# Performance work log

Hardware: AMD Instinct MI355X
Metric: run time of the kernel (lower is better)

The kernel has to match this reference:

```python
import jax, jax.numpy as jnp
import numpy as np

MASS, CHARGE, ALPHA, BETA = 1.0, 0.5, 0.1, 0.05
ETA = jnp.array([1.0, -1.0, -1.0, -1.0], dtype=jnp.float32)  # Minkowski metric diag


def setup_inputs() -> dict:
    key = jax.random.key(0)
    k1, k2, k3 = jax.random.split(key, 3)
    B = 262144
    y = jax.random.normal(k1, (B, 8), dtype=jnp.float32)
    W = jax.random.normal(k2, (4, 4), dtype=jnp.float32) * 0.3
    V = jax.random.normal(k3, (4, 4), dtype=jnp.float32) * 0.3
    return {"y": y, "W": W, "V": V}


def _lagrangian(z):
    # z = (x, u, A) concatenated, shape [12]
    x, u, A = z[0:4], z[4:8], z[8:12]
    kinetic = 0.5 * MASS * jnp.sum(ETA * u * u)
    coupling = CHARGE * jnp.sum(ETA * u * A)
    xu_term = ALPHA * jnp.sum((x * u) ** 2)      # makes J_xu nontrivial
    uA_term = BETA * jnp.sum(u * A) ** 2          # makes J_Au nontrivial
    return kinetic + coupling + xu_term + uA_term


def reference(y, W, V):
    def A_vec(x):  # vector potential A^mu(x), works on [4] or [B,4]
        return jnp.tanh(x @ W.T) + x @ V.T

    x = y[:, 0:4]   # [B,4] positions
    u = y[:, 4:8]   # [B,4] velocities
    A = A_vec(x)    # [B,4]
    z = jnp.concatenate([x, u, A], axis=1)  # [B,12] = (x,u,A)

    gradL = jax.vmap(jax.grad(_lagrangian))(z)      # [B,12]
    H = jax.vmap(jax.hessian(_lagrangian))(z)       # [B,12,12]

    dL_dx = gradL[:, 0:4]
    dL_dA = gradL[:, 8:12]
    J_xu = H[:, 0:4, 4:8]    # d^2L/(dx^mu du^nu)
    J_uu = H[:, 4:8, 4:8]    # d^2L/(du^mu du^nu)
    J_Au = H[:, 8:12, 4:8]   # d^2L/(dA^mu du^nu)

    # dA_dx[a, nu, i] = dA^i/dx^nu (matches tf.stack(..., axis=2) layout)
    jacA = jax.vmap(jax.jacfwd(A_vec))(x)           # [B, i, nu]
    dA_dx = jnp.transpose(jacA, (0, 2, 1))          # [B, nu, i]

    J_uu_inv = jnp.linalg.pinv(J_uu)                # [B,4,4]

    force = (dL_dx
             + jnp.einsum('ajk,ak->aj', dA_dx, dL_dA)
             - jnp.einsum('ai,aij->aj', u,
                          J_xu + jnp.einsum('ajk,akm->ajm', dA_dx, J_Au)))
    acceleration = jnp.einsum('ai,aij->aj', force, J_uu_inv)  # [B,4]
    return acceleration
```

## Files before the change

### kernel.cpp

```cpp
#include <hip/hip_runtime.h>
#include <math.h>


#define SIX_RCOND 2.86102294921875e-5
#define RCOND     4.76837158203125e-6

__device__ __forceinline__ void fast_tanh4(const double t[4], double th[4])
{
    const double LOG2E = 1.4426950408889634074;
    const double LN2HI = 6.93147180369123816490e-01;
    const double LN2LO = 1.90821492927058770002e-10;
    double e[4], opp[4];
    #pragma unroll
    for (int j = 0; j < 4; ++j) {
        double a  = fabs(t[j]);
        double z  = -2.0 * a;
        double zc = fmax(z, -64.0);
        double nf = rint(zc * LOG2E);
        double r  = fma(-nf, LN2HI, zc);
        r = fma(-nf, LN2LO, r);
        double p = 2.75573192239858906526e-07;
        p = fma(p, r, 2.75573192239858925110e-06);
        p = fma(p, r, 2.48015873015873015873e-05);
        p = fma(p, r, 1.98412698412698412698e-04);
        p = fma(p, r, 1.38888888888888888889e-03);
        p = fma(p, r, 8.33333333333333333333e-03);
        p = fma(p, r, 4.16666666666666666667e-02);
        p = fma(p, r, 1.66666666666666666667e-01);
        p = fma(p, r, 0.5);
        p = fma(p, r, 1.0);
        p = fma(p, r, 1.0);
        int n = (int)nf;
        double twon = __longlong_as_double(((long long)(1023 + n)) << 52);
        double ez = p * twon;
        ez = (z <= -40.0) ? 0.0 : ez;
        e[j]   = ez;
        opp[j] = 1.0 + ez;
    }
    double p01 = opp[0] * opp[1], p23 = opp[2] * opp[3];
    double rp  = 1.0 / (p01 * p23);
    double inv[4] = { opp[1] * p23 * rp, opp[0] * p23 * rp,
                      p01 * opp[3] * rp, p01 * opp[2] * rp };
    #pragma unroll
    for (int j = 0; j < 4; ++j)
        th[j] = copysign((1.0 - e[j]) * inv[j], t[j]);
}

__device__ __forceinline__ void model_terms(
    const double* sW, const double* sV,
    const double x[4], const double u[4],
    double A[4], double f[4], double d[4])
{
    const double eta[4] = {1.0, -1.0, -1.0, -1.0};
    const double CHG = 0.5, ALPHA = 0.1, BETA = 0.05;
    double t[4], s[4];
    #pragma unroll
    for (int j = 0; j < 4; ++j) {
        double tj = 0.0, sj = 0.0;
        #pragma unroll
        for (int k = 0; k < 4; ++k) {
            tj = fma(sW[j*4+k], x[k], tj);
            sj = fma(sV[j*4+k], x[k], sj);
        }
        t[j] = tj; s[j] = sj;
    }
    double th[4];
    fast_tanh4(t, th);
    double G[4][4];
    #pragma unroll
    for (int j = 0; j < 4; ++j) {
        A[j] = th[j] + s[j];
        double dth = 1.0 - th[j] * th[j];
        #pragma unroll
        for (int k = 0; k < 4; ++k) G[j][k] = fma(dth, sW[j*4+k], sV[j*4+k]);
    }
    double S = 0.0;
    #pragma unroll
    for (int k = 0; k < 4; ++k) S += u[k] * A[k];
    double P[4], R[4], Q[4];
    #pragma unroll
    for (int j = 0; j < 4; ++j) {
        double p = 0.0, r = 0.0, q = 0.0;
        #pragma unroll
        for (int k = 0; k < 4; ++k) {
            p += G[k][j] * u[k];
            r += G[j][k] * u[k];
            q += G[k][j] * (CHG * eta[k]) * u[k];
        }
        P[j] = p; R[j] = r; Q[j] = q;
    }
    double T = 0.0;
    #pragma unroll
    for (int j = 0; j < 4; ++j) T += u[j] * R[j];
    #pragma unroll
    for (int j = 0; j < 4; ++j) {
        f[j] = -2.0 * ALPHA * x[j] * u[j] * u[j]
             + Q[j]
             + 2.0 * BETA * S * P[j]
             - (CHG * eta[j] + 2.0 * BETA * S) * R[j]
             - 2.0 * BETA * A[j] * T;
        d[j] = eta[j] + 2.0 * ALPHA * x[j] * x[j];
    }
}

__device__ __forceinline__ void sm_solve_inv(
    const double invd[4], const double A[4], const double f[4], double acc[4])
{
    const double C2 = 0.1;
    double b[4], fd[4], den = 1.0, w = 0.0;
    #pragma unroll
    for (int j = 0; j < 4; ++j) {
        b[j]  = A[j] * invd[j];
        fd[j] = f[j] * invd[j];
        den  += C2 * A[j] * b[j];
        w    += b[j] * f[j];
    }
    double scale = C2 * w / den;
    #pragma unroll
    for (int j = 0; j < 4; ++j) acc[j] = fd[j] - b[j] * scale;
}

__device__ void jacobi_pinv_solve(
    const double d[4], const double A[4], const double f[4], double acc[4])
{
    const double C2 = 0.1;
    double M[4][4], Vm[4][4];
    #pragma unroll
    for (int r = 0; r < 4; ++r) {
        #pragma unroll
        for (int c = 0; c < 4; ++c) {
            M[r][c] = C2 * A[r] * A[c];
            Vm[r][c] = (r == c) ? 1.0 : 0.0;
        }
        M[r][r] += d[r];
    }
    for (int sweep = 0; sweep < 8; ++sweep) {
        #pragma unroll
        for (int p = 0; p < 3; ++p) {
            #pragma unroll
            for (int q2 = p + 1; q2 < 4; ++q2) {
                double apq = M[p][q2];
                if (fabs(apq) < 1e-280) continue;
                double app = M[p][p], aqq = M[q2][q2];
                double tau = (aqq - app) / (2.0 * apq);
                double tt = ((tau >= 0.0) ? 1.0 : -1.0) /
                            (fabs(tau) + sqrt(1.0 + tau * tau));
                double c = 1.0 / sqrt(1.0 + tt * tt);
                double s = tt * c;
                #pragma unroll
                for (int k = 0; k < 4; ++k) {
                    double mkp = M[k][p], mkq = M[k][q2];
                    M[k][p]  = c * mkp - s * mkq;
                    M[k][q2] = s * mkp + c * mkq;
                }
                #pragma unroll
                for (int k = 0; k < 4; ++k) {
                    double mpk = M[p][k], mqk = M[q2][k];
                    M[p][k]  = c * mpk - s * mqk;
                    M[q2][k] = s * mpk + c * mqk;
                }
                #pragma unroll
                for (int k = 0; k < 4; ++k) {
                    double vkp = Vm[k][p], vkq = Vm[k][q2];
                    Vm[k][p]  = c * vkp - s * vkq;
                    Vm[k][q2] = s * vkp + c * vkq;
                }
            }
        }
    }
    double lam[4], sigmax = 0.0;
    #pragma unroll
    for (int k = 0; k < 4; ++k) {
        lam[k] = M[k][k];
        double a = fabs(lam[k]);
        sigmax = (a > sigmax) ? a : sigmax;
    }
    double cutoff = RCOND * sigmax;
    #pragma unroll
    for (int j = 0; j < 4; ++j) acc[j] = 0.0;
    #pragma unroll
    for (int e = 0; e < 4; ++e) {
        if (fabs(lam[e]) > cutoff) {
            double coef = 0.0;
            #pragma unroll
            for (int k = 0; k < 4; ++k) coef += Vm[k][e] * f[k];
            coef /= lam[e];
            #pragma unroll
            for (int j = 0; j < 4; ++j) acc[j] += coef * Vm[j][e];
        }
    }
}

__global__ __launch_bounds__(256) void fast_kernel(
    const float* __restrict__ y, const float* __restrict__ W,
    const float* __restrict__ V, float* __restrict__ out,
    unsigned int* __restrict__ cnt, int* __restrict__ list,
    unsigned int cap, int B)
{
    __shared__ double sW[16], sV[16];
    if (threadIdx.x < 16)      sW[threadIdx.x]      = (double)W[threadIdx.x];
    else if (threadIdx.x < 32) sV[threadIdx.x - 16] = (double)V[threadIdx.x - 16];
    __syncthreads();

    int i = blockIdx.x * blockDim.x + threadIdx.x;
    if (i >= B) return;

    const float4* y4 = (const float4*)y;
    float4 xv = y4[2 * i];
    float4 uv = y4[2 * i + 1];
    double x[4] = {xv.x, xv.y, xv.z, xv.w};
    double u[4] = {uv.x, uv.y, uv.z, uv.w};

    double A[4], f[4], d[4];
    model_terms(sW, sV, x, u, A, f, d);

    const double C2 = 0.1;
    double mind = 1e300;
    #pragma unroll
    for (int j = 0; j < 4; ++j) {
        double a = fabs(d[j]);
        mind = (a < mind) ? a : mind;
    }
    double p01 = d[0] * d[1], p23 = d[2] * d[3];
    double prod = p01 * p23;
    double det = prod
        + C2 * (A[0]*A[0]*(d[1]*p23) + A[1]*A[1]*(d[0]*p23) +
                A[2]*A[2]*(p01*d[3]) + A[3]*A[3]*(p01*d[2]));
    double sumA2 = 0.0, sumA4 = 0.0, F2 = 0.0;
    #pragma unroll
    for (int j = 0; j < 4; ++j) {
        double Aj2 = A[j] * A[j];
        sumA2 += Aj2; sumA4 += Aj2 * Aj2;
        double Jjj = d[j] + C2 * Aj2;
        F2 += Jjj * Jjj;
    }
    F2 += C2 * C2 * (sumA2 * sumA2 - sumA4);
    double rowmax = 0.0;
    #pragma unroll
    for (int r = 0; r < 4; ++r) {
        double rs = 0.0;
        #pragma unroll
        for (int c = 0; c < 4; ++c) {
            double Jrc = C2 * A[r] * A[c] + ((r == c) ? d[r] : 0.0);
            rs += fabs(Jrc);
        }
        rowmax = (rs > rowmax) ? rs : rowmax;
    }
    double sig_hi2 = rowmax * rowmax;
    sig_hi2 = (F2 < sig_hi2) ? F2 : sig_hi2;
    bool safe = (fabs(det) > SIX_RCOND * sig_hi2 * sig_hi2) && (mind > 1e-3);

    if (safe) {
        double invprod = 1.0 / prod;
        double invd[4] = { d[1] * p23 * invprod, d[0] * p23 * invprod,
                           p01 * d[3] * invprod, p01 * d[2] * invprod };
        double acc[4];
        sm_solve_inv(invd, A, f, acc);
        float4 res;
        res.x = (float)acc[0]; res.y = (float)acc[1];
        res.z = (float)acc[2]; res.w = (float)acc[3];
        ((float4*)out)[i] = res;
    } else {
        unsigned int idx = atomicAdd(cnt, 1u);
        if (idx < cap) {
            list[idx] = i;
        } else {
            double invd[4] = { 1.0 / d[0], 1.0 / d[1], 1.0 / d[2], 1.0 / d[3] };
            double acc[4];
            sm_solve_inv(invd, A, f, acc);
            float4 res;
            res.x = (float)acc[0]; res.y = (float)acc[1];
            res.z = (float)acc[2]; res.w = (float)acc[3];
            ((float4*)out)[i] = res;
        }
    }
}

__global__ __launch_bounds__(256) void slow_kernel(
    const float* __restrict__ y, const float* __restrict__ W,
    const float* __restrict__ V, float* __restrict__ out,
    const unsigned int* __restrict__ cnt, const int* __restrict__ list,
    unsigned int cap)
{
    __shared__ double sW[16], sV[16];
    if (threadIdx.x < 16)      sW[threadIdx.x]      = (double)W[threadIdx.x];
    else if (threadIdx.x < 32) sV[threadIdx.x - 16] = (double)V[threadIdx.x - 16];
    __syncthreads();

    unsigned int n = *cnt;
    if (n > cap) n = cap;
    int stride = gridDim.x * blockDim.x;
    for (unsigned int j = blockIdx.x * blockDim.x + threadIdx.x; j < n; j += stride) {
        int i = list[j];
        const float4* y4 = (const float4*)y;
        float4 xv = y4[2 * i];
        float4 uv = y4[2 * i + 1];
        double x[4] = {xv.x, xv.y, xv.z, xv.w};
        double u[4] = {uv.x, uv.y, uv.z, uv.w};
        double A[4], f[4], d[4];
        model_terms(sW, sV, x, u, A, f, d);
        double acc[4];
        jacobi_pinv_solve(d, A, f, acc);
        float4 res;
        res.x = (float)acc[0]; res.y = (float)acc[1];
        res.z = (float)acc[2]; res.w = (float)acc[3];
        ((float4*)out)[i] = res;
    }
}

extern "C" void kernel_launch(void* const* d_in, const int* in_sizes, int n_in,
                              void* d_out, int out_size, void* d_ws, size_t ws_size,
                              hipStream_t stream) {
    const float* y = (const float*)d_in[0];
    const float* W = (const float*)d_in[1];
    const float* V = (const float*)d_in[2];
    float* out = (float*)d_out;
    int B = in_sizes[0] / 8;

    unsigned int* cnt = (unsigned int*)d_ws;
    int* list = (int*)((char*)d_ws + 16);
    unsigned int cap = (ws_size > 16) ? (unsigned int)((ws_size - 16) / sizeof(int)) : 0u;
    if (cap > (unsigned int)B) cap = (unsigned int)B;

    hipMemsetAsync(d_ws, 0, 16, stream);

    int block = 256;
    int grid = (B + block - 1) / block;
    fast_kernel<<<grid, block, 0, stream>>>(y, W, V, out, cnt, list, cap, B);
    slow_kernel<<<64, block, 0, stream>>>(y, W, V, out, cnt, list, cap);
}
```

Baseline: 83.18 us.

## Move fast-path Lagrangian force evaluation to fp32 with stricter safety filter

The fast kernel now computes the vector potential, tanh, Jacobian terms and the Sherman-Morrison solve in fp32, using the hardware exp2 and a Newton-refined reciprocal in place of the fp64 polynomial tanh and divisions. The safety test is loosened to a cheaper row-sum bound with a 1/1024 threshold, so more ill-conditioned rows get deferred to the slow kernel. There they are re-checked in fp64 and solved either by the fp64 Sherman-Morrison path or by the Jacobi pseudo-inverse. The slow kernel grid is doubled. The aim is to replace fp64 throughput on MI355X with fp32, at the cost of lower accuracy on the fast path and possibly more rows sent to the slow path.

```diff
diff --git a/kernel.cpp b/kernel.cpp
--- a/kernel.cpp
+++ b/kernel.cpp
@@ -4,6 +4,12 @@
 
 #define SIX_RCOND 2.86102294921875e-5
 #define RCOND     4.76837158203125e-6
+
+__device__ __forceinline__ float rcp_nr(float x) {
+    float r = __builtin_amdgcn_rcpf(x);
+    r = r * (2.0f - x * r);
+    return r;
+}
 
 __device__ __forceinline__ void fast_tanh4(const double t[4], double th[4])
 {
@@ -46,7 +52,7 @@
         th[j] = copysign((1.0 - e[j]) * inv[j], t[j]);
 }
 
-__device__ __forceinline__ void model_terms(
+__device__ __forceinline__ void model_terms_f64(
     const double* sW, const double* sV,
     const double x[4], const double u[4],
     double A[4], double f[4], double d[4])
@@ -103,15 +109,16 @@
     }
 }
 
-__device__ __forceinline__ void sm_solve_inv(
-    const double invd[4], const double A[4], const double f[4], double acc[4])
+__device__ __forceinline__ void sm_solve_f64(
+    const double d[4], const double A[4], const double f[4], double acc[4])
 {
     const double C2 = 0.1;
     double b[4], fd[4], den = 1.0, w = 0.0;
     #pragma unroll
     for (int j = 0; j < 4; ++j) {
-        b[j]  = A[j] * invd[j];
-        fd[j] = f[j] * invd[j];
+        double inv = 1.0 / d[j];
+        b[j]  = A[j] * inv;
+        fd[j] = f[j] * inv;
         den  += C2 * A[j] * b[j];
         w    += b[j] * f[j];
     }
@@ -197,9 +204,9 @@
     unsigned int* __restrict__ cnt, int* __restrict__ list,
     unsigned int cap, int B)
 {
-    __shared__ double sW[16], sV[16];
-    if (threadIdx.x < 16)      sW[threadIdx.x]      = (double)W[threadIdx.x];
-    else if (threadIdx.x < 32) sV[threadIdx.x - 16] = (double)V[threadIdx.x - 16];
+    __shared__ float sW[16], sV[16];
+    if (threadIdx.x < 16)      sW[threadIdx.x]      = W[threadIdx.x];
+    else if (threadIdx.x < 32) sV[threadIdx.x - 16] = V[threadIdx.x - 16];
     __syncthreads();
 
     int i = blockIdx.x * blockDim.x + threadIdx.x;
@@ -208,69 +215,125 @@
     const float4* y4 = (const float4*)y;
     float4 xv = y4[2 * i];
     float4 uv = y4[2 * i + 1];
-    double x[4] = {xv.x, xv.y, xv.z, xv.w};
-    double u[4] = {uv.x, uv.y, uv.z, uv.w};
-
-    double A[4], f[4], d[4];
-    model_terms(sW, sV, x, u, A, f, d);
-
-    const double C2 = 0.1;
-    double mind = 1e300;
-    #pragma unroll
-    for (int j = 0; j < 4; ++j) {
-        double a = fabs(d[j]);
-        mind = (a < mind) ? a : mind;
-    }
-    double p01 = d[0] * d[1], p23 = d[2] * d[3];
-    double prod = p01 * p23;
-    double det = prod
+    float x[4] = {xv.x, xv.y, xv.z, xv.w};
+    float u[4] = {uv.x, uv.y, uv.z, uv.w};
+
+    const float eta[4] = {1.0f, -1.0f, -1.0f, -1.0f};
+    const float CHG = 0.5f, ALPHA = 0.1f, BETA = 0.05f, C2 = 0.1f;
+    const float NEG2LOG2E = -2.8853900817779268f;
+
+    float t[4], sv[4];
+    #pragma unroll
+    for (int j = 0; j < 4; ++j) {
+        float tj = 0.0f, sj = 0.0f;
+        #pragma unroll
+        for (int k = 0; k < 4; ++k) {
+            tj = fmaf(sW[j*4+k], x[k], tj);
+            sj = fmaf(sV[j*4+k], x[k], sj);
+        }
+        t[j] = tj; sv[j] = sj;
+    }
+    float A[4], dth[4];
+    #pragma unroll
+    for (int j = 0; j < 4; ++j) {
+        float a  = fabsf(t[j]);
+        float e  = __builtin_amdgcn_exp2f(a * NEG2LOG2E);
+        float th = copysignf((1.0f - e) * rcp_nr(1.0f + e), t[j]);
+        A[j]   = th + sv[j];
+        dth[j] = 1.0f - th * th;
+    }
+    float G[4][4];
+    #pragma unroll
+    for (int j = 0; j < 4; ++j)
+        #pragma unroll
+        for (int k = 0; k < 4; ++k)
+            G[j][k] = fmaf(dth[j], sW[j*4+k], sV[j*4+k]);
+
+    float S = 0.0f;
+    #pragma unroll
+    for (int k = 0; k < 4; ++k) S = fmaf(u[k], A[k], S);
+    float P[4], R[4], Q[4];
+    #pragma unroll
+    for (int j = 0; j < 4; ++j) {
+        float p = 0.0f, r = 0.0f, q = 0.0f;
+        #pragma unroll
+        for (int k = 0; k < 4; ++k) {
+            p = fmaf(G[k][j], u[k], p);
+            r = fmaf(G[j][k], u[k], r);
+            q = fmaf(G[k][j] * (CHG * eta[k]), u[k], q);
+        }
+        P[j] = p; R[j] = r; Q[j] = q;
+    }
+    float T = 0.0f;
+    #pragma unroll
+    for (int j = 0; j < 4; ++j) T = fmaf(u[j], R[j], T);
+    float f[4], d[4];
+    #pragma unroll
+    for (int j = 0; j < 4; ++j) {
+        f[j] = -2.0f * ALPHA * x[j] * u[j] * u[j]
+             + Q[j]
+             + 2.0f * BETA * S * P[j]
+             - (CHG * eta[j] + 2.0f * BETA * S) * R[j]
+             - 2.0f * BETA * A[j] * T;
+        d[j] = eta[j] + 2.0f * ALPHA * x[j] * x[j];
+    }
+
+    float mind = fminf(fminf(fabsf(d[0]), fabsf(d[1])),
+                       fminf(fabsf(d[2]), fabsf(d[3])));
+    float p01 = d[0] * d[1], p23 = d[2] * d[3];
+    float prod = p01 * p23;
+    float det = prod
         + C2 * (A[0]*A[0]*(d[1]*p23) + A[1]*A[1]*(d[0]*p23) +
                 A[2]*A[2]*(p01*d[3]) + A[3]*A[3]*(p01*d[2]));
-    double sumA2 = 0.0, sumA4 = 0.0, F2 = 0.0;
-    #pragma unroll
-    for (int j = 0; j < 4; ++j) {
-        double Aj2 = A[j] * A[j];
-        sumA2 += Aj2; sumA4 += Aj2 * Aj2;
-        double Jjj = d[j] + C2 * Aj2;
-        F2 += Jjj * Jjj;
-    }
-    F2 += C2 * C2 * (sumA2 * sumA2 - sumA4);
-    double rowmax = 0.0;
+    float rowmax = 0.0f;
     #pragma unroll
     for (int r = 0; r < 4; ++r) {
-        double rs = 0.0;
+        float rs = 0.0f;
         #pragma unroll
         for (int c = 0; c < 4; ++c) {
-            double Jrc = C2 * A[r] * A[c] + ((r == c) ? d[r] : 0.0);
-            rs += fabs(Jrc);
-        }
-        rowmax = (rs > rowmax) ? rs : rowmax;
-    }
-    double sig_hi2 = rowmax * rowmax;
-    sig_hi2 = (F2 < sig_hi2) ? F2 : sig_hi2;
-    bool safe = (fabs(det) > SIX_RCOND * sig_hi2 * sig_hi2) && (mind > 1e-3);
+            float Jrc = C2 * A[r] * A[c] + ((r == c) ? d[r] : 0.0f);
+            rs += fabsf(Jrc);
+        }
+        rowmax = fmaxf(rs, rowmax);
+    }
+    float sig2 = rowmax * rowmax;
+    bool safe = (fabsf(det) > sig2 * sig2 * (1.0f / 1024.0f)) && (mind > 1e-3f);
 
     if (safe) {
-        double invprod = 1.0 / prod;
-        double invd[4] = { d[1] * p23 * invprod, d[0] * p23 * invprod,
-                           p01 * d[3] * invprod, p01 * d[2] * invprod };
-        double acc[4];
-        sm_solve_inv(invd, A, f, acc);
+        float invprod = rcp_nr(prod);
+        float invd[4] = { d[1] * p23 * invprod, d[0] * p23 * invprod,
+                          p01 * d[3] * invprod, p01 * d[2] * invprod };
+        float b[4], fd[4], den = 1.0f, w = 0.0f;
+        #pragma unroll
+        for (int j = 0; j < 4; ++j) {
+            b[j]  = A[j] * invd[j];
+            fd[j] = f[j] * invd[j];
+            den   = fmaf(C2 * A[j], b[j], den);
+            w     = fmaf(b[j], f[j], w);
+        }
+        float scale = (C2 * w) * rcp_nr(den);
         float4 res;
-        res.x = (float)acc[0]; res.y = (float)acc[1];
-        res.z = (float)acc[2]; res.w = (float)acc[3];
+        res.x = fd[0] - b[0] * scale; res.y = fd[1] - b[1] * scale;
+        res.z = fd[2] - b[2] * scale; res.w = fd[3] - b[3] * scale;
         ((float4*)out)[i] = res;
     } else {
         unsigned int idx = atomicAdd(cnt, 1u);
         if (idx < cap) {
             list[idx] = i;
         } else {
-            double invd[4] = { 1.0 / d[0], 1.0 / d[1], 1.0 / d[2], 1.0 / d[3] };
-            double acc[4];
-            sm_solve_inv(invd, A, f, acc);
+            float b[4], fd[4], den = 1.0f, w = 0.0f;
+            #pragma unroll
+            for (int j = 0; j < 4; ++j) {
+                float inv = rcp_nr(d[j]);
+                b[j]  = A[j] * inv;
+                fd[j] = f[j] * inv;
+                den   = fmaf(C2 * A[j], b[j], den);
+                w     = fmaf(b[j], f[j], w);
+            }
+            float scale = (C2 * w) * rcp_nr(den);
             float4 res;
-            res.x = (float)acc[0]; res.y = (float)acc[1];
-            res.z = (float)acc[2]; res.w = (float)acc[3];
+            res.x = fd[0] - b[0] * scale; res.y = fd[1] - b[1] * scale;
+            res.z = fd[2] - b[2] * scale; res.w = fd[3] - b[3] * scale;
             ((float4*)out)[i] = res;
         }
     }
@@ -298,9 +361,47 @@
         double x[4] = {xv.x, xv.y, xv.z, xv.w};
         double u[4] = {uv.x, uv.y, uv.z, uv.w};
         double A[4], f[4], d[4];
-        model_terms(sW, sV, x, u, A, f, d);
+        model_terms_f64(sW, sV, x, u, A, f, d);
+
+        const double C2 = 0.1;
+        double mind = 1e300;
+        #pragma unroll
+        for (int jj = 0; jj < 4; ++jj) {
+            double a = fabs(d[jj]);
+            mind = (a < mind) ? a : mind;
+        }
+        double p01 = d[0] * d[1], p23 = d[2] * d[3];
+        double det = p01 * p23
+            + C2 * (A[0]*A[0]*(d[1]*p23) + A[1]*A[1]*(d[0]*p23) +
+                    A[2]*A[2]*(p01*d[3]) + A[3]*A[3]*(p01*d[2]));
+        double sumA2 = 0.0, sumA4 = 0.0, F2 = 0.0;
+        #pragma unroll
+        for (int jj = 0; jj < 4; ++jj) {
+            double Aj2 = A[jj] * A[jj];
+            sumA2 += Aj2; sumA4 += Aj2 * Aj2;
+            double Jjj = d[jj] + C2 * Aj2;
+            F2 += Jjj * Jjj;
+        }
+        F2 += C2 * C2 * (sumA2 * sumA2 - sumA4);
+        double rowmax = 0.0;
+        #pragma unroll
+        for (int r = 0; r < 4; ++r) {
+            double rs = 0.0;
+            #pragma unroll
+            for (int c = 0; c < 4; ++c) {
+                double Jrc = C2 * A[r] * A[c] + ((r == c) ? d[r] : 0.0);
+                rs += fabs(Jrc);
+            }
+            rowmax = (rs > rowmax) ? rs : rowmax;
+        }
+        double sig_hi2 = rowmax * rowmax;
+        sig_hi2 = (F2 < sig_hi2) ? F2 : sig_hi2;
+        bool safe = (fabs(det) > SIX_RCOND * sig_hi2 * sig_hi2) && (mind > 1e-3);
+
         double acc[4];
-        jacobi_pinv_solve(d, A, f, acc);
+        if (safe) sm_solve_f64(d, A, f, acc);
+        else      jacobi_pinv_solve(d, A, f, acc);
+
         float4 res;
         res.x = (float)acc[0]; res.y = (float)acc[1];
         res.z = (float)acc[2]; res.w = (float)acc[3];
@@ -327,5 +428,5 @@
     int block = 256;
     int grid = (B + block - 1) / block;
     fast_kernel<<<grid, block, 0, stream>>>(y, W, V, out, cnt, list, cap, B);
-    slow_kernel<<<64, block, 0, stream>>>(y, W, V, out, cnt, list, cap);
-}
+    slow_kernel<<<128, block, 0, stream>>>(y, W, V, out, cnt, list, cap);
+}
```

Measured after the change: 120.7 us. 45.1% more time.
